# Performance work log

Measured on AMD Instinct MI355X. Metric: run time of the kernel, lower is better.

## Reference

```python
import jax, jax.numpy as jnp
import numpy as np

B, N, C, H = 4, 1024, 256, 8
HD = C // H
SCALE = HD ** -0.5


def setup_inputs() -> dict:
    key = jax.random.key(0)
    ks = jax.random.split(key, 8)
    x = jax.random.normal(ks[0], (B, N, C), jnp.float32)
    voxel_coord = jax.random.uniform(ks[1], (B, N, 3), jnp.float32)
    # Linear weights stored as [in, out] so y = x @ W + b (same math as torch x @ W.T)
    W_qk = jax.random.normal(ks[2], (C, 2 * C), jnp.float32) * 0.02
    W_v = jax.random.normal(ks[3], (C, C), jnp.float32) * 0.02
    W_proj = jax.random.normal(ks[4], (C, C), jnp.float32) * 0.02
    b_proj = jnp.zeros((C,), jnp.float32)
    W_pos = jax.random.normal(ks[5], (4, H), jnp.float32) * 0.02
    b_pos = jnp.zeros((H,), jnp.float32)
    gating = jnp.ones((H,), jnp.float32)
    return dict(x=x, voxel_coord=voxel_coord, W_qk=W_qk, W_v=W_v,
                W_proj=W_proj, b_proj=b_proj, W_pos=W_pos, b_pos=b_pos,
                gating=gating)


def reference(x, voxel_coord, W_qk, W_v, W_proj, b_proj, W_pos, b_pos, gating):
    b, n, c = x.shape
    # Relative 3D positional encoding: positions[b,i,j] = p[j] - p[i]; feature = [dx,dy,dz,dist]
    diff = voxel_coord[:, None, :, :] - voxel_coord[:, :, None, :]          # [B,N,N,3]
    dist = jnp.sqrt(jnp.sum(diff * diff, axis=-1, keepdims=True))           # [B,N,N,1]
    rel = jnp.concatenate([diff, dist], axis=-1)                            # [B,N,N,4]

    # Positional score per head, softmax over keys j
    pos_logits = jnp.einsum('bijf,fh->bhij', rel, W_pos) + b_pos[None, :, None, None]
    pos_score = jax.nn.softmax(pos_logits, axis=-1)                         # [B,H,N,N]

    # Content score: SDPA with V = I  ==  plain softmax attention matrix
    qk = (x @ W_qk).reshape(b, n, 2, H, HD)
    q = jnp.transpose(qk[:, :, 0], (0, 2, 1, 3))                            # [B,H,N,hd]
    k = jnp.transpose(qk[:, :, 1], (0, 2, 1, 3))
    patch_score = jax.nn.softmax(jnp.einsum('bhid,bhjd->bhij', q, k) * SCALE, axis=-1)

    # Gated mix + renormalize
    sig = jax.nn.sigmoid(gating)[None, :, None, None]
    attn = (1.0 - sig) * patch_score + sig * pos_score
    attn = attn / jnp.sum(attn, axis=-1, keepdims=True)

    v = (x @ W_v).reshape(b, n, H, HD).transpose(0, 2, 1, 3)                # [B,H,N,hd]
    out = jnp.einsum('bhij,bhjd->bihd', attn, v).reshape(b, n, c)           # [B,N,C]
    out = out @ W_proj + b_proj
    return out
```

## Files before the change

### kernel.cpp

```cpp
#include <hip/hip_runtime.h>
#include <hip/hip_bf16.h>

#define LOG2E 1.4426950408889634f

typedef __attribute__((ext_vector_type(8))) short bf16x8_t;
typedef __attribute__((ext_vector_type(4))) float f32x4_t;

#if __has_builtin(__builtin_amdgcn_exp2f)
#define EXP2F_(x) __builtin_amdgcn_exp2f(x)
#else
__device__ __forceinline__ float EXP2F_(float x) {
    float r; asm volatile("v_exp_f32 %0, %1\ns_nop 1" : "=v"(r) : "v"(x)); return r;
}
#endif
#if __has_builtin(__builtin_amdgcn_sqrtf)
#define SQRTF_(x) __builtin_amdgcn_sqrtf(x)
#else
__device__ __forceinline__ float SQRTF_(float x) {
    float r; asm volatile("v_sqrt_f32 %0, %1\ns_nop 1" : "=v"(r) : "v"(x)); return r;
}
#endif

__device__ __forceinline__ unsigned short f2bf(float f) {
    unsigned u = __float_as_uint(f);
    u += 0x7fffu + ((u >> 16) & 1u);
    return (unsigned short)(u >> 16);
}

__device__ __forceinline__ unsigned pk2(float lo, float hi) {
    union { __hip_bfloat162 h2; unsigned u; } cvt;
    cvt.h2 = __float22bfloat162_rn(make_float2(lo, hi));
    return cvt.u;
}

__device__ __forceinline__ void stage16(const unsigned short* g, unsigned short* l, int lane) {
#if __has_builtin(__builtin_amdgcn_global_load_lds)
    __builtin_amdgcn_global_load_lds((const __attribute__((address_space(1))) void*)g,
                                     (__attribute__((address_space(3))) void*)l, 16, 0, 0);
#else
    *(uint4*)((char*)l + lane * 16) = *(const uint4*)g;
#endif
}

__global__ __launch_bounds__(256) void k_convert(
    const float* __restrict__ Wqk, const float* __restrict__ Wv,
    const float* __restrict__ Wpj,
    unsigned short* __restrict__ Wqk_t, unsigned short* __restrict__ Wv_t,
    unsigned short* __restrict__ Wp_t)
{
    __shared__ unsigned short T[64 * 72];
    const int bid = blockIdx.x, tid = threadIdx.x;
    const float* src; unsigned short* dst; int N_, kt, nt;
    if (bid < 32)      { src = Wqk; dst = Wqk_t; N_ = 512; kt = bid & 3; nt = bid >> 2; }
    else if (bid < 48) { int t = bid - 32; src = Wv;  dst = Wv_t; N_ = 256; kt = t & 3; nt = t >> 2; }
    else               { int t = bid - 48; src = Wpj; dst = Wp_t; N_ = 256; kt = t & 3; nt = t >> 2; }
    const int kr = tid >> 2, seg = tid & 3;
    #pragma unroll
    for (int u = 0; u < 4; ++u) {
        float4 v = *(const float4*)(src + (kt * 64 + kr) * N_ + nt * 64 + seg * 16 + u * 4);
        T[(seg * 16 + u * 4 + 0) * 72 + kr] = f2bf(v.x);
        T[(seg * 16 + u * 4 + 1) * 72 + kr] = f2bf(v.y);
        T[(seg * 16 + u * 4 + 2) * 72 + kr] = f2bf(v.z);
        T[(seg * 16 + u * 4 + 3) * 72 + kr] = f2bf(v.w);
    }
    __syncthreads();
    const int n = tid >> 2, s2 = tid & 3;
    uint4 a = *(uint4*)&T[n * 72 + s2 * 16];
    uint4 b2 = *(uint4*)&T[n * 72 + s2 * 16 + 8];
    *(uint4*)(dst + (nt * 64 + n) * 256 + kt * 64 + s2 * 16) = a;
    *(uint4*)(dst + (nt * 64 + n) * 256 + kt * 64 + s2 * 16 + 8) = b2;
}

__global__ __launch_bounds__(256) void k_qkv(
    const float* __restrict__ x,
    const unsigned short* __restrict__ Wqk_t,
    const unsigned short* __restrict__ Wv_t,
    unsigned short* __restrict__ q_ws, unsigned short* __restrict__ k_ws,
    unsigned short* __restrict__ v_ws)
{
    __shared__ unsigned short Al[64 * 64];
    __shared__ unsigned short Bl[64 * 64];
    const int tid = threadIdx.x;
    const int n0 = blockIdx.x * 64;
    const int row0 = blockIdx.y * 64;
    const int w = tid >> 6, lane = tid & 63;
    const int lhi = lane >> 4, llo = lane & 15;
    const unsigned short* Bsrc = (n0 < 512) ? (Wqk_t + n0 * 256) : (Wv_t + (n0 - 512) * 256);

    const int sr = lane >> 3, sc = lane & 7;
    const int scx = sc ^ sr;

    f32x4_t acc[4] = {};
    for (int kc = 0; kc < 4; ++kc) {
        #pragma unroll
        for (int s = 0; s < 2; ++s) {
            int chunk = w * 2 + s;
            int r = chunk * 8 + sr;
            const float* ax = x + (row0 + r) * 256 + kc * 64 + scx * 8;
            float4 a0 = *(const float4*)ax, a1 = *(const float4*)(ax + 4);
            uint4 pk;
            pk.x = pk2(a0.x, a0.y); pk.y = pk2(a0.z, a0.w);
            pk.z = pk2(a1.x, a1.y); pk.w = pk2(a1.z, a1.w);
            *(uint4*)(&Al[r * 64 + sc * 8]) = pk;
            stage16(Bsrc + r * 256 + kc * 64 + scx * 8, &Bl[chunk * 512], lane);
        }
        __syncthreads();
        #pragma unroll
        for (int ks = 0; ks < 2; ++ks) {
            int ua = ((ks * 4 + lhi) ^ (llo & 7)) * 8;
            bf16x8_t a = *(const bf16x8_t*)(&Al[(w * 16 + llo) * 64 + ua]);
            #pragma unroll
            for (int nt = 0; nt < 4; ++nt) {
                bf16x8_t b = *(const bf16x8_t*)(&Bl[(nt * 16 + llo) * 64 + ua]);
                acc[nt] = __builtin_amdgcn_mfma_f32_16x16x32_bf16(a, b, acc[nt], 0, 0, 0);
            }
        }
        __syncthreads();
    }
    constexpr float QSC = (float)(1.4426950408889634 / 5.656854249492380195206754896838);
    #pragma unroll
    for (int nt = 0; nt < 4; ++nt) {
        int ng = n0 + nt * 16 + llo;
        #pragma unroll
        for (int r = 0; r < 4; ++r) {
            int ig = row0 + w * 16 + lhi * 4 + r;
            float val = acc[nt][r];
            int b = ig >> 10, i = ig & 1023;
            if (ng < 256) {
                int h = ng >> 5, d = ng & 31;
                q_ws[((b * 8 + h) * 1024 + i) * 32 + d] = f2bf(val * QSC);
            } else if (ng < 512) {
                int c = ng - 256, h = c >> 5, d = c & 31;
                k_ws[((b * 8 + h) * 1024 + i) * 32 + d] = f2bf(val);
            } else {
                int c = ng - 512, h = c >> 5, d = c & 31;
                v_ws[((b * 8 + h) * 1024 + i) * 32 + d] = f2bf(val);
            }
        }
    }
}

__global__ __launch_bounds__(512, 6) void k_attn(
    const unsigned short* __restrict__ q_ws,
    const unsigned short* __restrict__ k_ws,
    const unsigned short* __restrict__ v_ws,
    const float* __restrict__ coords,
    const float* __restrict__ W_pos,
    const float* __restrict__ b_pos,
    const float* __restrict__ gating,
    unsigned short* __restrict__ o_ws)
{
    __shared__ unsigned short Kl[2 * 64 * 32];
    __shared__ unsigned short Vt[2 * 32 * 64];
    __shared__ unsigned short Wp[2 * 64 * 64];
    __shared__ unsigned short Wq[2 * 64 * 64];
    __shared__ float4 TX[128];
    __shared__ float  TA[128];

    const int tid = threadIdx.x;
    const int bid = blockIdx.x;
    const int xcd = bid & 7, s = bid >> 3;
    const int bh = xcd * 4 + (s >> 4);
    const int it = s & 15;
    const int b = bh >> 3, h = bh & 7;

    const int w = tid >> 6, lane = tid & 63;
    const int wi = w & 3, wj = w >> 2;
    const int lhi = lane >> 4, llo = lane & 15;

    const float wxl = W_pos[0 * 8 + h] * LOG2E;
    const float wyl = W_pos[1 * 8 + h] * LOG2E;
    const float wzl = W_pos[2 * 8 + h] * LOG2E;
    const float wdl = W_pos[3 * 8 + h] * LOG2E;
    const float bpl = b_pos[h] * LOG2E;

    const int i_base = it * 64 + wi * 16;
    bf16x8_t qf = *(const bf16x8_t*)(q_ws + (bh * 1024 + i_base + llo) * 32 + lhi * 8);

    const float* cb_ = coords + b * 3072;
    const int ig = i_base + llo;
    float xi = cb_[ig * 3 + 0], yi = cb_[ig * 3 + 1], zi = cb_[ig * 3 + 2];
    float si = fmaf(xi, xi, fmaf(yi, yi, zi * zi));
    float cil = fmaf(wzl, zi, fmaf(wyl, yi, wxl * xi));

    bf16x8_t ones;
    #pragma unroll
    for (int e = 0; e < 8; ++e) ones[e] = (short)0x3F80;

    f32x4_t accP[2] = {}, accQ[2] = {};
    f32x4_t accLp = {}, accLq = {};

    const int jhbase = wj * 512;
    const int wc = w & 3;

    for (int t = 0; t < 8; ++t) {
        const int j0s = (w >> 2) * 512 + t * 64;
        stage16(k_ws + (bh * 1024 + j0s + wc * 16 + (lane >> 2)) * 32 + (lane & 3) * 8,
                &Kl[(w >> 2) * 2048 + wc * 512], lane);
        {
            uint4 vv = *(const uint4*)(v_ws + (bh * 1024 + j0s + lane) * 32 + wc * 8);
            const unsigned short* pv = (const unsigned short*)&vv;
            #pragma unroll
            for (int e = 0; e < 8; ++e)
                Vt[((w >> 2) * 32 + wc * 8 + e) * 64 + (((lane >> 3) ^ e) * 8) + (lane & 7)] = pv[e];
        }
        if (tid < 128) {
            int half = tid >> 6, jl = tid & 63;
            int jg = half * 512 + t * 64 + jl;
            float xj = cb_[jg * 3 + 0], yj = cb_[jg * 3 + 1], zj = cb_[jg * 3 + 2];
            TX[half * 64 + jl] = make_float4(xj, yj, zj, fmaf(xj, xj, fmaf(yj, yj, zj * zj)));
            TA[half * 64 + jl] = fmaf(wzl, zj, fmaf(wyl, yj, wxl * xj)) + bpl;
        }
        __syncthreads();

        #pragma unroll
        for (int jq = 0; jq < 4; ++jq) {
            bf16x8_t kf = *(const bf16x8_t*)(&Kl[wj * 2048 + (jq * 16 + llo) * 32 + lhi * 8]);
            f32x4_t zero = {};
            f32x4_t sv = __builtin_amdgcn_mfma_f32_16x16x32_bf16(kf, qf, zero, 0, 0, 0);
            int jlb = wj * 64 + jq * 16 + lhi * 4;
            float ep[4], eq[4];
            #pragma unroll
            for (int r = 0; r < 4; ++r) {
                float4 cj = TX[jlb + r];
                float aj = TA[jlb + r];
                float dot = fmaf(cj.x, xi, fmaf(cj.y, yi, cj.z * zi));
                float d2 = fmaf(-2.0f, dot, si + cj.w);
                float dist = SQRTF_(d2);
                float spos = fmaf(wdl, dist, aj - cil);
                ep[r] = EXP2F_(sv[r]);
                eq[r] = EXP2F_(spos);
            }
            int row = wj * 64 + wi * 16 + llo;
            int off = row * 64 + (((jq * 2 + (lhi >> 1)) ^ (llo & 7)) * 8) + (lhi & 1) * 4;
            uint2 uP, uQ;
            uP.x = pk2(ep[0], ep[1]); uP.y = pk2(ep[2], ep[3]);
            uQ.x = pk2(eq[0], eq[1]); uQ.y = pk2(eq[2], eq[3]);
            *(uint2*)(&Wp[off]) = uP;
            *(uint2*)(&Wq[off]) = uQ;
        }

        #pragma unroll
        for (int jb = 0; jb < 2; ++jb) {
            int uu = ((jb * 4 + lhi) ^ (llo & 7)) * 8;
            bf16x8_t bP = *(const bf16x8_t*)(&Wp[(wj * 64 + wi * 16 + llo) * 64 + uu]);
            bf16x8_t bQ = *(const bf16x8_t*)(&Wq[(wj * 64 + wi * 16 + llo) * 64 + uu]);
            accLp = __builtin_amdgcn_mfma_f32_16x16x32_bf16(ones, bP, accLp, 0, 0, 0);
            accLq = __builtin_amdgcn_mfma_f32_16x16x32_bf16(ones, bQ, accLq, 0, 0, 0);
            #pragma unroll
            for (int dt = 0; dt < 2; ++dt) {
                bf16x8_t af = *(const bf16x8_t*)(&Vt[(wj * 32 + dt * 16 + llo) * 64 + uu]);
                accP[dt] = __builtin_amdgcn_mfma_f32_16x16x32_bf16(af, bP, accP[dt], 0, 0, 0);
                accQ[dt] = __builtin_amdgcn_mfma_f32_16x16x32_bf16(af, bQ, accQ[dt], 0, 0, 0);
            }
        }
        __syncthreads();
    }

    float* red = (float*)Wp;
    float* LPQ = (float*)Wq;
    if (wj == 1) {
        float* pr = red + (wi * 64 + lane) * 16;
        *(f32x4_t*)(pr + 0) = accP[0]; *(f32x4_t*)(pr + 4)  = accP[1];
        *(f32x4_t*)(pr + 8) = accQ[0]; *(f32x4_t*)(pr + 12) = accQ[1];
        if (lhi == 0) { LPQ[wi * 16 + llo] = accLp[0]; LPQ[64 + wi * 16 + llo] = accLq[0]; }
    }
    __syncthreads();
    if (wj == 0) {
        const float* pr = red + (wi * 64 + lane) * 16;
        float Lp = accLp[0] + LPQ[wi * 16 + llo];
        float Lq = accLq[0] + LPQ[64 + wi * 16 + llo];
        float sig = 1.0f / (1.0f + __expf(-gating[h]));
        float ca = (1.0f - sig) / Lp, cb2 = sig / Lq;
        int rowg = b * 1024 + it * 64 + wi * 16 + llo;
        #pragma unroll
        for (int dt = 0; dt < 2; ++dt) {
            float o0 = ca * (accP[dt][0] + pr[dt * 4 + 0]) + cb2 * (accQ[dt][0] + pr[8 + dt * 4 + 0]);
            float o1 = ca * (accP[dt][1] + pr[dt * 4 + 1]) + cb2 * (accQ[dt][1] + pr[8 + dt * 4 + 1]);
            float o2 = ca * (accP[dt][2] + pr[dt * 4 + 2]) + cb2 * (accQ[dt][2] + pr[8 + dt * 4 + 2]);
            float o3 = ca * (accP[dt][3] + pr[dt * 4 + 3]) + cb2 * (accQ[dt][3] + pr[8 + dt * 4 + 3]);
            uint2 uu;
            uu.x = pk2(o0, o1); uu.y = pk2(o2, o3);
            *(uint2*)(o_ws + (size_t)rowg * 256 + h * 32 + dt * 16 + lhi * 4) = uu;
        }
    }
}

__global__ __launch_bounds__(256) void k_proj(
    const unsigned short* __restrict__ A,
    const unsigned short* __restrict__ Bt,
    const float* __restrict__ bias,
    float* __restrict__ out)
{
    __shared__ unsigned short Al[64 * 64];
    __shared__ unsigned short Bl[64 * 64];
    const int tid = threadIdx.x;
    const int n0 = blockIdx.x * 64;
    const int row0 = blockIdx.y * 64;
    const int w = tid >> 6, lane = tid & 63;
    const int lhi = lane >> 4, llo = lane & 15;
    const int sr = lane >> 3, sc = lane & 7;
    const int scx = sc ^ sr;

    f32x4_t acc[4] = {};
    for (int kc = 0; kc < 4; ++kc) {
        #pragma unroll
        for (int s = 0; s < 2; ++s) {
            int chunk = w * 2 + s;
            int r = chunk * 8 + sr;
            stage16(A + (row0 + r) * 256 + kc * 64 + scx * 8, &Al[chunk * 512], lane);
            stage16(Bt + (n0 + r) * 256 + kc * 64 + scx * 8, &Bl[chunk * 512], lane);
        }
        __syncthreads();
        #pragma unroll
        for (int ks = 0; ks < 2; ++ks) {
            int ua = ((ks * 4 + lhi) ^ (llo & 7)) * 8;
            bf16x8_t a = *(const bf16x8_t*)(&Al[(w * 16 + llo) * 64 + ua]);
            #pragma unroll
            for (int nt = 0; nt < 4; ++nt) {
                bf16x8_t b = *(const bf16x8_t*)(&Bl[(nt * 16 + llo) * 64 + ua]);
                acc[nt] = __builtin_amdgcn_mfma_f32_16x16x32_bf16(a, b, acc[nt], 0, 0, 0);
            }
        }
        __syncthreads();
    }
    #pragma unroll
    for (int nt = 0; nt < 4; ++nt) {
        int ng = n0 + nt * 16 + llo;
        float bv = bias[ng];
        #pragma unroll
        for (int r = 0; r < 4; ++r) {
            int ig = row0 + w * 16 + lhi * 4 + r;
            out[ig * 256 + ng] = acc[nt][r] + bv;
        }
    }
}

extern "C" void kernel_launch(void* const* d_in, const int* in_sizes, int n_in,
                              void* d_out, int out_size, void* d_ws, size_t ws_size,
                              hipStream_t stream)
{
    const float* x    = (const float*)d_in[0];
    const float* vc   = (const float*)d_in[1];
    const float* Wqk  = (const float*)d_in[2];
    const float* Wv   = (const float*)d_in[3];
    const float* Wpj  = (const float*)d_in[4];
    const float* bpj  = (const float*)d_in[5];
    const float* Wpos = (const float*)d_in[6];
    const float* bpos = (const float*)d_in[7];
    const float* gat  = (const float*)d_in[8];
    float* out = (float*)d_out;

    char* ws = (char*)d_ws;
    unsigned short* Wqk_t = (unsigned short*)(ws + 0);
    unsigned short* Wv_t  = (unsigned short*)(ws + 262144);
    unsigned short* Wp_t  = (unsigned short*)(ws + 393216);
    unsigned short* q_ws  = (unsigned short*)(ws + 524288);
    unsigned short* k_ws  = (unsigned short*)(ws + 2621440);
    unsigned short* v_ws  = (unsigned short*)(ws + 4718592);
    unsigned short* o_ws  = (unsigned short*)(ws + 6815744);

    hipLaunchKernelGGL(k_convert, dim3(64), dim3(256), 0, stream,
                       Wqk, Wv, Wpj, Wqk_t, Wv_t, Wp_t);
    hipLaunchKernelGGL(k_qkv, dim3(12, 64), dim3(256), 0, stream,
                       x, Wqk_t, Wv_t, q_ws, k_ws, v_ws);
    hipLaunchKernelGGL(k_attn, dim3(512), dim3(512), 0, stream,
                       q_ws, k_ws, v_ws, vc, Wpos, bpos, gat, o_ws);
    hipLaunchKernelGGL(k_proj, dim3(4, 64), dim3(256), 0, stream,
                       o_ws, Wp_t, bpj, out);
}
```

Baseline: 123.7 us.

## Precompute per-head coord table, pre-tile V, use LDS transpose reads in attention

Adds a per-(batch,head) float4 table of coordinates plus the W_pos-projected term, built in the weight-conversion kernel, so the attention kernel no longer recomputes it per tile. V is stored pre-tiled so it can be staged with direct global-to-LDS loads, replacing the per-element transposing LDS stores. The positional exponentials are computed with a different lane-to-element mapping (8 query rows per lane, direct distance instead of the expanded dot form), written to per-wave LDS and read back with ds_read_b64_tr_b16 transpose loads. Launch bounds drop from 6 to 2 waves hint, which may raise register use and lower occupancy; the extra per-lane register arrays and explicit lgkmcnt waits add their own costs.

New measurement: 117.5 us. 1.05x faster.

```diff
diff --git a/kernel.cpp b/kernel.cpp
--- a/kernel.cpp
+++ b/kernel.cpp
@@ -5,6 +5,7 @@
 
 typedef __attribute__((ext_vector_type(8))) short bf16x8_t;
 typedef __attribute__((ext_vector_type(4))) float f32x4_t;
+typedef __attribute__((ext_vector_type(4))) short s16x4_t;
 
 #if __has_builtin(__builtin_amdgcn_exp2f)
 #define EXP2F_(x) __builtin_amdgcn_exp2f(x)
@@ -42,33 +43,61 @@
 #endif
 }
 
+__device__ __forceinline__ unsigned lds_off(const void* p) {
+    return (unsigned)(size_t)(const __attribute__((address_space(3))) void*)p;
+}
+
+__device__ __forceinline__ s16x4_t TR16(unsigned addr) {
+    s16x4_t r;
+    asm volatile("ds_read_b64_tr_b16 %0, %1" : "=v"(r) : "v"(addr) : "memory");
+    return r;
+}
+__device__ __forceinline__ void tr_fence() {
+    asm volatile("s_waitcnt lgkmcnt(0)" ::: "memory");
+    __builtin_amdgcn_sched_barrier(0);
+}
+
 __global__ __launch_bounds__(256) void k_convert(
     const float* __restrict__ Wqk, const float* __restrict__ Wv,
-    const float* __restrict__ Wpj,
+    const float* __restrict__ Wpj, const float* __restrict__ coords,
+    const float* __restrict__ W_pos,
     unsigned short* __restrict__ Wqk_t, unsigned short* __restrict__ Wv_t,
-    unsigned short* __restrict__ Wp_t)
+    unsigned short* __restrict__ Wp_t, float4* __restrict__ tbl)
 {
     __shared__ unsigned short T[64 * 72];
     const int bid = blockIdx.x, tid = threadIdx.x;
-    const float* src; unsigned short* dst; int N_, kt, nt;
-    if (bid < 32)      { src = Wqk; dst = Wqk_t; N_ = 512; kt = bid & 3; nt = bid >> 2; }
-    else if (bid < 48) { int t = bid - 32; src = Wv;  dst = Wv_t; N_ = 256; kt = t & 3; nt = t >> 2; }
-    else               { int t = bid - 48; src = Wpj; dst = Wp_t; N_ = 256; kt = t & 3; nt = t >> 2; }
-    const int kr = tid >> 2, seg = tid & 3;
-    #pragma unroll
-    for (int u = 0; u < 4; ++u) {
-        float4 v = *(const float4*)(src + (kt * 64 + kr) * N_ + nt * 64 + seg * 16 + u * 4);
-        T[(seg * 16 + u * 4 + 0) * 72 + kr] = f2bf(v.x);
-        T[(seg * 16 + u * 4 + 1) * 72 + kr] = f2bf(v.y);
-        T[(seg * 16 + u * 4 + 2) * 72 + kr] = f2bf(v.z);
-        T[(seg * 16 + u * 4 + 3) * 72 + kr] = f2bf(v.w);
-    }
-    __syncthreads();
-    const int n = tid >> 2, s2 = tid & 3;
-    uint4 a = *(uint4*)&T[n * 72 + s2 * 16];
-    uint4 b2 = *(uint4*)&T[n * 72 + s2 * 16 + 8];
-    *(uint4*)(dst + (nt * 64 + n) * 256 + kt * 64 + s2 * 16) = a;
-    *(uint4*)(dst + (nt * 64 + n) * 256 + kt * 64 + s2 * 16 + 8) = b2;
+    if (bid < 64) {
+        const float* src; unsigned short* dst; int N_, kt, nt;
+        if (bid < 32)      { src = Wqk; dst = Wqk_t; N_ = 512; kt = bid & 3; nt = bid >> 2; }
+        else if (bid < 48) { int t = bid - 32; src = Wv;  dst = Wv_t; N_ = 256; kt = t & 3; nt = t >> 2; }
+        else               { int t = bid - 48; src = Wpj; dst = Wp_t; N_ = 256; kt = t & 3; nt = t >> 2; }
+        const int kr = tid >> 2, seg = tid & 3;
+        #pragma unroll
+        for (int u = 0; u < 4; ++u) {
+            float4 v = *(const float4*)(src + (kt * 64 + kr) * N_ + nt * 64 + seg * 16 + u * 4);
+            T[(seg * 16 + u * 4 + 0) * 72 + kr] = f2bf(v.x);
+            T[(seg * 16 + u * 4 + 1) * 72 + kr] = f2bf(v.y);
+            T[(seg * 16 + u * 4 + 2) * 72 + kr] = f2bf(v.z);
+            T[(seg * 16 + u * 4 + 3) * 72 + kr] = f2bf(v.w);
+        }
+        __syncthreads();
+        const int n = tid >> 2, s2 = tid & 3;
+        uint4 a = *(uint4*)&T[n * 72 + s2 * 16];
+        uint4 b2 = *(uint4*)&T[n * 72 + s2 * 16 + 8];
+        *(uint4*)(dst + (nt * 64 + n) * 256 + kt * 64 + s2 * 16) = a;
+        *(uint4*)(dst + (nt * 64 + n) * 256 + kt * 64 + s2 * 16 + 8) = b2;
+    } else {
+        const int bh = bid - 64, b = bh >> 3, h = bh & 7;
+        const float wxl = W_pos[0 * 8 + h] * LOG2E;
+        const float wyl = W_pos[1 * 8 + h] * LOG2E;
+        const float wzl = W_pos[2 * 8 + h] * LOG2E;
+        for (int jl = tid; jl < 1024; jl += 256) {
+            float x = coords[(b * 1024 + jl) * 3 + 0];
+            float y = coords[(b * 1024 + jl) * 3 + 1];
+            float z = coords[(b * 1024 + jl) * 3 + 2];
+            tbl[bh * 1024 + jl] = make_float4(x, y, z, fmaf(wxl, x, fmaf(wyl, y, wzl * z)));
+        }
+    }
 }
 
 __global__ __launch_bounds__(256) void k_qkv(
@@ -134,28 +163,27 @@
                 k_ws[((b * 8 + h) * 1024 + i) * 32 + d] = f2bf(val);
             } else {
                 int c = ng - 512, h = c >> 5, d = c & 31;
-                v_ws[((b * 8 + h) * 1024 + i) * 32 + d] = f2bf(val);
+                v_ws[(size_t)(b * 8 + h) * 32768 +
+                     ((i >> 2) * 2 + (d >> 4)) * 64 + (i & 3) * 16 + (d & 15)] = f2bf(val);
             }
         }
     }
 }
 
-__global__ __launch_bounds__(512, 6) void k_attn(
+__global__ __launch_bounds__(512, 2) void k_attn(
     const unsigned short* __restrict__ q_ws,
     const unsigned short* __restrict__ k_ws,
     const unsigned short* __restrict__ v_ws,
-    const float* __restrict__ coords,
+    const float4* __restrict__ tbl,
     const float* __restrict__ W_pos,
     const float* __restrict__ b_pos,
     const float* __restrict__ gating,
     unsigned short* __restrict__ o_ws)
 {
-    __shared__ unsigned short Kl[2 * 64 * 32];
-    __shared__ unsigned short Vt[2 * 32 * 64];
-    __shared__ unsigned short Wp[2 * 64 * 64];
-    __shared__ unsigned short Wq[2 * 64 * 64];
-    __shared__ float4 TX[128];
-    __shared__ float  TA[128];
+    __shared__ __align__(16) unsigned short Kl[2 * 64 * 32];
+    __shared__ __align__(16) unsigned short Vt[2 * 64 * 32];
+    __shared__ __align__(16) unsigned short Wp[2 * 64 * 64];
+    __shared__ __align__(16) unsigned short Eq[8 * 64 * 16];
 
     const int tid = threadIdx.x;
     const int bid = blockIdx.x;
@@ -168,20 +196,24 @@
     const int wi = w & 3, wj = w >> 2;
     const int lhi = lane >> 4, llo = lane & 15;
 
-    const float wxl = W_pos[0 * 8 + h] * LOG2E;
-    const float wyl = W_pos[1 * 8 + h] * LOG2E;
-    const float wzl = W_pos[2 * 8 + h] * LOG2E;
     const float wdl = W_pos[3 * 8 + h] * LOG2E;
     const float bpl = b_pos[h] * LOG2E;
 
     const int i_base = it * 64 + wi * 16;
     bf16x8_t qf = *(const bf16x8_t*)(q_ws + (bh * 1024 + i_base + llo) * 32 + lhi * 8);
 
-    const float* cb_ = coords + b * 3072;
-    const int ig = i_base + llo;
-    float xi = cb_[ig * 3 + 0], yi = cb_[ig * 3 + 1], zi = cb_[ig * 3 + 2];
-    float si = fmaf(xi, xi, fmaf(yi, yi, zi * zi));
-    float cil = fmaf(wzl, zi, fmaf(wyl, yi, wxl * xi));
+    const float4* tb4 = tbl + (size_t)bh * 1024;
+    float xi8[8], yi8[8], zi8[8], ci8[8];
+    const bool hsel = (lane & 1);
+    #pragma unroll
+    for (int e = 0; e < 8; ++e) {
+        float4 lo = tb4[i_base + e];
+        float4 hi = tb4[i_base + 8 + e];
+        xi8[e] = hsel ? hi.x : lo.x;
+        yi8[e] = hsel ? hi.y : lo.y;
+        zi8[e] = hsel ? hi.z : lo.z;
+        ci8[e] = hsel ? hi.w : lo.w;
+    }
 
     bf16x8_t ones;
     #pragma unroll
@@ -190,75 +222,82 @@
     f32x4_t accP[2] = {}, accQ[2] = {};
     f32x4_t accLp = {}, accLq = {};
 
-    const int jhbase = wj * 512;
-    const int wc = w & 3;
+    const int jl1 = ((lane >> 3) << 2) + ((lane & 7) >> 1);
+    unsigned short* eqw = &Eq[w * 1024];
+    const unsigned eqbase = lds_off(&Eq[w * 1024]) + lhi * 256 + llo * 8;
+    const unsigned vtbase = lds_off(&Vt[wj * 2048]) + lhi * 512 + llo * 8;
 
     for (int t = 0; t < 8; ++t) {
-        const int j0s = (w >> 2) * 512 + t * 64;
-        stage16(k_ws + (bh * 1024 + j0s + wc * 16 + (lane >> 2)) * 32 + (lane & 3) * 8,
-                &Kl[(w >> 2) * 2048 + wc * 512], lane);
+        const int j0 = wj * 512 + t * 64;
+        stage16(k_ws + (bh * 1024 + j0 + wi * 16 + (lane >> 2)) * 32 + (lane & 3) * 8,
+                &Kl[wj * 2048 + wi * 512], lane);
+        stage16(v_ws + (size_t)bh * 32768 + j0 * 32 + wi * 512 + lane * 8,
+                &Vt[wj * 2048 + wi * 512], lane);
+        float4 t1 = tb4[j0 + jl1];
+        float4 t2 = tb4[j0 + jl1 + 32];
+        __syncthreads();
+
         {
-            uint4 vv = *(const uint4*)(v_ws + (bh * 1024 + j0s + lane) * 32 + wc * 8);
-            const unsigned short* pv = (const unsigned short*)&vv;
+            float aj1 = t1.w + bpl, aj2 = t2.w + bpl;
+            float eq1[8], eq2[8];
             #pragma unroll
-            for (int e = 0; e < 8; ++e)
-                Vt[((w >> 2) * 32 + wc * 8 + e) * 64 + (((lane >> 3) ^ e) * 8) + (lane & 7)] = pv[e];
-        }
-        if (tid < 128) {
-            int half = tid >> 6, jl = tid & 63;
-            int jg = half * 512 + t * 64 + jl;
-            float xj = cb_[jg * 3 + 0], yj = cb_[jg * 3 + 1], zj = cb_[jg * 3 + 2];
-            TX[half * 64 + jl] = make_float4(xj, yj, zj, fmaf(xj, xj, fmaf(yj, yj, zj * zj)));
-            TA[half * 64 + jl] = fmaf(wzl, zj, fmaf(wyl, yj, wxl * xj)) + bpl;
-        }
-        __syncthreads();
+            for (int e = 0; e < 8; ++e) {
+                float dx = t1.x - xi8[e], dy = t1.y - yi8[e], dz = t1.z - zi8[e];
+                float d2 = fmaf(dx, dx, fmaf(dy, dy, dz * dz));
+                eq1[e] = EXP2F_(fmaf(wdl, SQRTF_(d2), aj1 - ci8[e]));
+                float ex = t2.x - xi8[e], ey = t2.y - yi8[e], ez = t2.z - zi8[e];
+                float e2 = fmaf(ex, ex, fmaf(ey, ey, ez * ez));
+                eq2[e] = EXP2F_(fmaf(wdl, SQRTF_(e2), aj2 - ci8[e]));
+            }
+            uint4 u1, u2;
+            u1.x = pk2(eq1[0], eq1[1]); u1.y = pk2(eq1[2], eq1[3]);
+            u1.z = pk2(eq1[4], eq1[5]); u1.w = pk2(eq1[6], eq1[7]);
+            u2.x = pk2(eq2[0], eq2[1]); u2.y = pk2(eq2[2], eq2[3]);
+            u2.z = pk2(eq2[4], eq2[5]); u2.w = pk2(eq2[6], eq2[7]);
+            *(uint4*)(&eqw[lane * 8]) = u1;
+            *(uint4*)(&eqw[512 + lane * 8]) = u2;
+        }
 
         #pragma unroll
         for (int jq = 0; jq < 4; ++jq) {
             bf16x8_t kf = *(const bf16x8_t*)(&Kl[wj * 2048 + (jq * 16 + llo) * 32 + lhi * 8]);
             f32x4_t zero = {};
             f32x4_t sv = __builtin_amdgcn_mfma_f32_16x16x32_bf16(kf, qf, zero, 0, 0, 0);
-            int jlb = wj * 64 + jq * 16 + lhi * 4;
-            float ep[4], eq[4];
-            #pragma unroll
-            for (int r = 0; r < 4; ++r) {
-                float4 cj = TX[jlb + r];
-                float aj = TA[jlb + r];
-                float dot = fmaf(cj.x, xi, fmaf(cj.y, yi, cj.z * zi));
-                float d2 = fmaf(-2.0f, dot, si + cj.w);
-                float dist = SQRTF_(d2);
-                float spos = fmaf(wdl, dist, aj - cil);
-                ep[r] = EXP2F_(sv[r]);
-                eq[r] = EXP2F_(spos);
-            }
-            int row = wj * 64 + wi * 16 + llo;
-            int off = row * 64 + (((jq * 2 + (lhi >> 1)) ^ (llo & 7)) * 8) + (lhi & 1) * 4;
-            uint2 uP, uQ;
-            uP.x = pk2(ep[0], ep[1]); uP.y = pk2(ep[2], ep[3]);
-            uQ.x = pk2(eq[0], eq[1]); uQ.y = pk2(eq[2], eq[3]);
+            float ep0 = EXP2F_(sv[0]), ep1 = EXP2F_(sv[1]);
+            float ep2 = EXP2F_(sv[2]), ep3 = EXP2F_(sv[3]);
+            int off = (wj * 64 + wi * 16 + llo) * 64 +
+                      (((jq * 2 + (lhi >> 1)) ^ (llo & 7)) * 8) + (lhi & 1) * 4;
+            uint2 uP;
+            uP.x = pk2(ep0, ep1); uP.y = pk2(ep2, ep3);
             *(uint2*)(&Wp[off]) = uP;
-            *(uint2*)(&Wq[off]) = uQ;
         }
 
         #pragma unroll
         for (int jb = 0; jb < 2; ++jb) {
             int uu = ((jb * 4 + lhi) ^ (llo & 7)) * 8;
             bf16x8_t bP = *(const bf16x8_t*)(&Wp[(wj * 64 + wi * 16 + llo) * 64 + uu]);
-            bf16x8_t bQ = *(const bf16x8_t*)(&Wq[(wj * 64 + wi * 16 + llo) * 64 + uu]);
+            s16x4_t q0 = TR16(eqbase + jb * 1024);
+            s16x4_t q1 = TR16(eqbase + jb * 1024 + 128);
+            s16x4_t a00 = TR16(vtbase + jb * 2048 + 0);
+            s16x4_t a01 = TR16(vtbase + jb * 2048 + 256);
+            s16x4_t a10 = TR16(vtbase + jb * 2048 + 128);
+            s16x4_t a11 = TR16(vtbase + jb * 2048 + 384);
+            tr_fence();
+            bf16x8_t bQ  = __builtin_shufflevector(q0, q1, 0, 1, 2, 3, 4, 5, 6, 7);
+            bf16x8_t af0 = __builtin_shufflevector(a00, a01, 0, 1, 2, 3, 4, 5, 6, 7);
+            bf16x8_t af1 = __builtin_shufflevector(a10, a11, 0, 1, 2, 3, 4, 5, 6, 7);
             accLp = __builtin_amdgcn_mfma_f32_16x16x32_bf16(ones, bP, accLp, 0, 0, 0);
             accLq = __builtin_amdgcn_mfma_f32_16x16x32_bf16(ones, bQ, accLq, 0, 0, 0);
-            #pragma unroll
-            for (int dt = 0; dt < 2; ++dt) {
-                bf16x8_t af = *(const bf16x8_t*)(&Vt[(wj * 32 + dt * 16 + llo) * 64 + uu]);
-                accP[dt] = __builtin_amdgcn_mfma_f32_16x16x32_bf16(af, bP, accP[dt], 0, 0, 0);
-                accQ[dt] = __builtin_amdgcn_mfma_f32_16x16x32_bf16(af, bQ, accQ[dt], 0, 0, 0);
-            }
+            accP[0] = __builtin_amdgcn_mfma_f32_16x16x32_bf16(af0, bP, accP[0], 0, 0, 0);
+            accQ[0] = __builtin_amdgcn_mfma_f32_16x16x32_bf16(af0, bQ, accQ[0], 0, 0, 0);
+            accP[1] = __builtin_amdgcn_mfma_f32_16x16x32_bf16(af1, bP, accP[1], 0, 0, 0);
+            accQ[1] = __builtin_amdgcn_mfma_f32_16x16x32_bf16(af1, bQ, accQ[1], 0, 0, 0);
         }
         __syncthreads();
     }
 
     float* red = (float*)Wp;
-    float* LPQ = (float*)Wq;
+    float* LPQ = (float*)Eq;
     if (wj == 1) {
         float* pr = red + (wi * 64 + lane) * 16;
         *(f32x4_t*)(pr + 0) = accP[0]; *(f32x4_t*)(pr + 4)  = accP[1];
@@ -359,13 +398,14 @@
     unsigned short* k_ws  = (unsigned short*)(ws + 2621440);
     unsigned short* v_ws  = (unsigned short*)(ws + 4718592);
     unsigned short* o_ws  = (unsigned short*)(ws + 6815744);
-
-    hipLaunchKernelGGL(k_convert, dim3(64), dim3(256), 0, stream,
-                       Wqk, Wv, Wpj, Wqk_t, Wv_t, Wp_t);
+    float4*         tbl   = (float4*)(ws + 8912896);
+
+    hipLaunchKernelGGL(k_convert, dim3(96), dim3(256), 0, stream,
+                       Wqk, Wv, Wpj, vc, Wpos, Wqk_t, Wv_t, Wp_t, tbl);
     hipLaunchKernelGGL(k_qkv, dim3(12, 64), dim3(256), 0, stream,
                        x, Wqk_t, Wv_t, q_ws, k_ws, v_ws);
     hipLaunchKernelGGL(k_attn, dim3(512), dim3(512), 0, stream,
-                       q_ws, k_ws, v_ws, vc, Wpos, bpos, gat, o_ws);
+                       q_ws, k_ws, v_ws, tbl, Wpos, bpos, gat, o_ws);
     hipLaunchKernelGGL(k_proj, dim3(4, 64), dim3(256), 0, stream,
                        o_ws, Wp_t, bpj, out);
 }
```
